# Performance work log

Hardware: AMD Instinct MI355X
Metric: run time of the kernel (lower is better)

The kernel has to match this reference:

```python
import jax, jax.numpy as jnp
import numpy as np
from jax import lax


def setup_inputs() -> dict:
    key = jax.random.key(0)
    k1, k2 = jax.random.split(key)
    B, C, H, W = 4, 32, 512, 512
    x = jax.random.normal(k1, (B, C, H, W), dtype=jnp.float32)
    # offset conv params: out_ch = 2*k*k = 18 (init: small weights, zero bias)
    w_off = jax.random.normal(k2, (18, C, 3, 3), dtype=jnp.float32) * 0.05
    b_off = jnp.zeros((18,), dtype=jnp.float32)
    return {"x": x, "w_off": w_off, "b_off": b_off}


def _grid_sample_bilinear_zeros(x, grid):
    # x: (B,C,H,W); grid: (B,H,W,2) in [-1,1], align_corners=True, zeros padding
    B, C, H, W = x.shape
    ix = (grid[..., 0] + 1.0) * 0.5 * (W - 1)  # (B,H,W)
    iy = (grid[..., 1] + 1.0) * 0.5 * (H - 1)
    x0 = jnp.floor(ix); y0 = jnp.floor(iy)
    x1 = x0 + 1.0;      y1 = y0 + 1.0
    wx1 = ix - x0; wx0 = 1.0 - wx1
    wy1 = iy - y0; wy0 = 1.0 - wy1
    bi = jnp.arange(B)[:, None, None]

    def corner(yc, xc, w):
        valid = (xc >= 0) & (xc <= W - 1) & (yc >= 0) & (yc <= H - 1)
        xi = jnp.clip(xc, 0, W - 1).astype(jnp.int32)
        yi = jnp.clip(yc, 0, H - 1).astype(jnp.int32)
        v = x[bi, :, yi, xi]  # (B,H,W,C)
        return v * (w * valid.astype(x.dtype))[..., None]

    out = (corner(y0, x0, wy0 * wx0) + corner(y0, x1, wy0 * wx1)
           + corner(y1, x0, wy1 * wx0) + corner(y1, x1, wy1 * wx1))
    return out.transpose(0, 3, 1, 2)  # (B,C,H,W)


def reference(x, w_off, b_off):
    B, C, H, W = x.shape
    # offset conv: 3x3, stride 1, padding 1 (shape-preserving)
    off = lax.conv_general_dilated(
        x, w_off, window_strides=(1, 1), padding=((1, 1), (1, 1)),
        dimension_numbers=("NCHW", "OIHW", "NCHW"))
    off = off + b_off[None, :, None, None]               # (B,18,H,W)
    off = off.transpose(0, 2, 3, 1).reshape(B, H, W, 9, 2)
    # base integer grid: (x, y) per pixel
    gy, gx = jnp.meshgrid(jnp.arange(H, dtype=x.dtype),
                          jnp.arange(W, dtype=x.dtype), indexing="ij")
    base = jnp.stack([gx, gy], axis=-1)                  # (H,W,2)
    g = base[None, :, :, None, :] + off                  # (B,H,W,9,2)
    g = g / jnp.array([W - 1, H - 1], dtype=x.dtype) * 2.0 - 1.0
    g = g[:, :, :, 0, :]                                 # only first kernel offset used
    return _grid_sample_bilinear_zeros(x, g)
```

## Files before the change

kernel.cpp:

```cpp
#include <hip/hip_runtime.h>

#define BB 4
#define CC 32
#define HH 512
#define WW 512
#define PLANE ((size_t)HH * WW)

typedef float fx4 __attribute__((ext_vector_type(4)));

__global__ __launch_bounds__(256) void deform_fused_kernel(
    const float* __restrict__ x, const float* __restrict__ w_off,
    const float* __restrict__ b_off, float* __restrict__ out) {
  const int nb = gridDim.x;
  const int i  = blockIdx.x;
  const int j  = (i & 7) * (nb >> 3) + (i >> 3);
  const int b    = j >> 8;
  const int row0 = (j & 255) << 1;

  const int t    = threadIdx.x;
  const int w4   = (t & 127) << 2;
  const int h    = row0 + (t >> 7);
  const int lane = t & 63;

  float4 a0v, a1v;
  a0v.x = a0v.y = a0v.z = a0v.w = b_off[0];
  a1v.x = a1v.y = a1v.z = a1v.w = b_off[1];

  const float* xb = x + (size_t)b * CC * PLANE + (size_t)h * WW + w4;

  float4 mA[3], mB[3];
  float  eA[3], eB[3];

  auto load_ch = [&](int ci, float4* m, float* e) {
#pragma unroll
    for (int r = 0; r < 3; ++r) {
      const int hy = h - 1 + r;
      const float* q = xb + (size_t)ci * PLANE + (ptrdiff_t)(r - 1) * WW;
      if (hy >= 0 && hy < HH) {
        m[r] = *(const float4*)q;
        const float* ea = (lane == 0) ? q - 1 : q + 4;
        const bool eok = (lane == 0) ? (w4 > 0)
                                     : (lane == 63 && w4 < WW - 4);
        e[r] = eok ? *ea : 0.f;
      } else {
        m[r].x = m[r].y = m[r].z = m[r].w = 0.f;
        e[r] = 0.f;
      }
    }
  };

  auto compute_ch = [&](int ci, const float4* m, const float* e) {
    const float* wp0 = w_off + ci * 9;
    const float* wp1 = w_off + 288 + ci * 9;
#pragma unroll
    for (int kh = 0; kh < 3; ++kh) {
      float vl = __shfl_up(m[kh].w, 1);
      if (lane == 0) vl = e[kh];
      float vr = __shfl_down(m[kh].x, 1);
      if (lane == 63) vr = e[kh];
      const float a0 = wp0[kh * 3 + 0], a1 = wp0[kh * 3 + 1], a2 = wp0[kh * 3 + 2];
      const float c0 = wp1[kh * 3 + 0], c1 = wp1[kh * 3 + 1], c2 = wp1[kh * 3 + 2];
      a0v.x += vl * a0 + m[kh].x * a1 + m[kh].y * a2;
      a0v.y += m[kh].x * a0 + m[kh].y * a1 + m[kh].z * a2;
      a0v.z += m[kh].y * a0 + m[kh].z * a1 + m[kh].w * a2;
      a0v.w += m[kh].z * a0 + m[kh].w * a1 + vr * a2;
      a1v.x += vl * c0 + m[kh].x * c1 + m[kh].y * c2;
      a1v.y += m[kh].x * c0 + m[kh].y * c1 + m[kh].z * c2;
      a1v.z += m[kh].y * c0 + m[kh].z * c1 + m[kh].w * c2;
      a1v.w += m[kh].z * c0 + m[kh].w * c1 + vr * c2;
    }
  };

  load_ch(0, mA, eA);
  for (int ci = 0; ci < CC - 2; ci += 2) {
    load_ch(ci + 1, mB, eB);
    compute_ch(ci, mA, eA);
    load_ch(ci + 2, mA, eA);
    compute_ch(ci + 1, mB, eB);
  }
  load_ch(CC - 1, mB, eB);
  compute_ch(CC - 2, mA, eA);
  compute_ch(CC - 1, mB, eB);

  float A0[4], A1[4], B0[4], B1[4];
  int   r0[4], r1[4];
  const float offx[4] = {a0v.x, a0v.y, a0v.z, a0v.w};
  const float offy[4] = {a1v.x, a1v.y, a1v.z, a1v.w};
#pragma unroll
  for (int p = 0; p < 4; ++p) {
    const float ix = (float)(w4 + p) + offx[p];
    const float iy = (float)h + offy[p];
    const float x0f = floorf(ix);
    const float y0f = floorf(iy);
    const float wx1 = ix - x0f, wx0 = 1.f - wx1;
    const float wy1 = iy - y0f, wy0 = 1.f - wy1;
    const bool vx0 = (x0f >= 0.f) && (x0f <= (float)(WW - 1));
    const bool vx1 = (x0f + 1.f >= 0.f) && (x0f + 1.f <= (float)(WW - 1));
    const bool vy0 = (y0f >= 0.f) && (y0f <= (float)(HH - 1));
    const bool vy1 = (y0f + 1.f >= 0.f) && (y0f + 1.f <= (float)(HH - 1));
    const int xi0 = (int)fminf(fmaxf(x0f, 0.f), (float)(WW - 1));
    const int xi1 = (int)fminf(fmaxf(x0f + 1.f, 0.f), (float)(WW - 1));
    const int yi0 = (int)fminf(fmaxf(y0f, 0.f), (float)(HH - 1));
    const int yi1 = (int)fminf(fmaxf(y0f + 1.f, 0.f), (float)(HH - 1));
    const float w00 = wy0 * wx0 * ((vy0 && vx0) ? 1.f : 0.f);
    const float w01 = wy0 * wx1 * ((vy0 && vx1) ? 1.f : 0.f);
    const float w10 = wy1 * wx0 * ((vy1 && vx0) ? 1.f : 0.f);
    const float w11 = wy1 * wx1 * ((vy1 && vx1) ? 1.f : 0.f);
    const int xL = (int)fminf(fmaxf(x0f, 0.f), (float)(WW - 2));
    const int s0 = (xi0 > xL) ? 1 : 0;
    const int s1 = (xi1 > xL) ? 1 : 0;
    A0[p] = (s0 ? 0.f : w00) + (s1 ? 0.f : w01);
    A1[p] = (s0 ? w00 : 0.f) + (s1 ? w01 : 0.f);
    B0[p] = (s0 ? 0.f : w10) + (s1 ? 0.f : w11);
    B1[p] = (s0 ? w10 : 0.f) + (s1 ? w11 : 0.f);
    r0[p] = yi0 * WW + xL;
    r1[p] = yi1 * WW + xL;
  }

  const float* xp = x + (size_t)b * CC * PLANE;
  float* ob = out + (size_t)b * CC * PLANE + (size_t)h * WW + w4;

#pragma unroll 1
  for (int cg = 0; cg < 8; ++cg) {
    float2 t0[4][4], t1[4][4];
    const float* pc = xp;
#pragma unroll
    for (int c = 0; c < 4; ++c) {
#pragma unroll
      for (int p = 0; p < 4; ++p) {
        __builtin_memcpy(&t0[c][p], pc + r0[p], 8);
        __builtin_memcpy(&t1[c][p], pc + r1[p], 8);
      }
      pc += PLANE;
    }
    float* o = ob;
#pragma unroll
    for (int c = 0; c < 4; ++c) {
      fx4 v;
      v.x = t0[c][0].x * A0[0] + t0[c][0].y * A1[0] + t1[c][0].x * B0[0] + t1[c][0].y * B1[0];
      v.y = t0[c][1].x * A0[1] + t0[c][1].y * A1[1] + t1[c][1].x * B0[1] + t1[c][1].y * B1[1];
      v.z = t0[c][2].x * A0[2] + t0[c][2].y * A1[2] + t1[c][2].x * B0[2] + t1[c][2].y * B1[2];
      v.w = t0[c][3].x * A0[3] + t0[c][3].y * A1[3] + t1[c][3].x * B0[3] + t1[c][3].y * B1[3];
      __builtin_nontemporal_store(v, (fx4*)o);
      o += PLANE;
    }
    xp += (size_t)4 * PLANE;
    ob += (size_t)4 * PLANE;
  }
}

extern "C" void kernel_launch(void* const* d_in, const int* in_sizes, int n_in,
                              void* d_out, int out_size, void* d_ws, size_t ws_size,
                              hipStream_t stream) {
  const float* x     = (const float*)d_in[0];
  const float* w_off = (const float*)d_in[1];
  const float* b_off = (const float*)d_in[2];
  float* out = (float*)d_out;

  deform_fused_kernel<<<1024, 256, 0, stream>>>(x, w_off, b_off, out);
}
```

Before: 298.4 us.

## Halve per-thread pixel work to two pixels and double block count

Each thread now handles 2 adjacent pixels instead of 4, and each 256-thread block covers one full row instead of two half-rows, with the grid doubled to 2048 blocks. A launch-bounds occupancy hint of 6 is added. The aim is lower register use and more waves in flight to hide gather latency. The cost is narrower float2 loads and stores, more wavefront-edge shuffles per pixel, and recomputed weight loads per block.

```diff
diff --git a/kernel.cpp b/kernel.cpp
--- a/kernel.cpp
+++ b/kernel.cpp
@@ -6,68 +6,63 @@
 #define WW 512
 #define PLANE ((size_t)HH * WW)
 
-typedef float fx4 __attribute__((ext_vector_type(4)));
+typedef float fx2 __attribute__((ext_vector_type(2)));
 
-__global__ __launch_bounds__(256) void deform_fused_kernel(
+__global__ __launch_bounds__(256, 6) void deform_fused_kernel(
     const float* __restrict__ x, const float* __restrict__ w_off,
     const float* __restrict__ b_off, float* __restrict__ out) {
   const int nb = gridDim.x;
   const int i  = blockIdx.x;
   const int j  = (i & 7) * (nb >> 3) + (i >> 3);
-  const int b    = j >> 8;
-  const int row0 = (j & 255) << 1;
+  const int b  = j >> 9;
+  const int h  = j & 511;
 
   const int t    = threadIdx.x;
-  const int w4   = (t & 127) << 2;
-  const int h    = row0 + (t >> 7);
+  const int w2   = t << 1;
   const int lane = t & 63;
 
-  float4 a0v, a1v;
-  a0v.x = a0v.y = a0v.z = a0v.w = b_off[0];
-  a1v.x = a1v.y = a1v.z = a1v.w = b_off[1];
+  float2 a0v, a1v;
+  a0v.x = a0v.y = b_off[0];
+  a1v.x = a1v.y = b_off[1];
 
-  const float* xb = x + (size_t)b * CC * PLANE + (size_t)h * WW + w4;
+  const float* xb = x + (size_t)b * CC * PLANE + (size_t)h * WW + w2;
 
-  float4 mA[3], mB[3];
+  float2 mA[3], mB[3];
   float  eA[3], eB[3];
 
-  auto load_ch = [&](int ci, float4* m, float* e) {
+  auto load_ch = [&](int ci, float2* m, float* e) {
 #pragma unroll
     for (int r = 0; r < 3; ++r) {
       const int hy = h - 1 + r;
       const float* q = xb + (size_t)ci * PLANE + (ptrdiff_t)(r - 1) * WW;
       if (hy >= 0 && hy < HH) {
-        m[r] = *(const float4*)q;
-        const float* ea = (lane == 0) ? q - 1 : q + 4;
-        const bool eok = (lane == 0) ? (w4 > 0)
-                                     : (lane == 63 && w4 < WW - 4);
+        m[r] = *(const float2*)q;
+        const float* ea = (lane == 0) ? q - 1 : q + 2;
+        const bool eok = (lane == 0) ? (w2 > 0)
+                                     : (lane == 63 && w2 < WW - 2);
         e[r] = eok ? *ea : 0.f;
       } else {
-        m[r].x = m[r].y = m[r].z = m[r].w = 0.f;
+        m[r].x = m[r].y = 0.f;
         e[r] = 0.f;
       }
     }
   };
 
-  auto compute_ch = [&](int ci, const float4* m, const float* e) {
+  auto compute_ch = [&](int ci, const float2* m, const float* e) {
     const float* wp0 = w_off + ci * 9;
     const float* wp1 = w_off + 288 + ci * 9;
 #pragma unroll
     for (int kh = 0; kh < 3; ++kh) {
-      float vl = __shfl_up(m[kh].w, 1);
+      float vl = __shfl_up(m[kh].y, 1);
       if (lane == 0) vl = e[kh];
       float vr = __shfl_down(m[kh].x, 1);
       if (lane == 63) vr = e[kh];
       const float a0 = wp0[kh * 3 + 0], a1 = wp0[kh * 3 + 1], a2 = wp0[kh * 3 + 2];
       const float c0 = wp1[kh * 3 + 0], c1 = wp1[kh * 3 + 1], c2 = wp1[kh * 3 + 2];
       a0v.x += vl * a0 + m[kh].x * a1 + m[kh].y * a2;
-      a0v.y += m[kh].x * a0 + m[kh].y * a1 + m[kh].z * a2;
-      a0v.z += m[kh].y * a0 + m[kh].z * a1 + m[kh].w * a2;
-      a0v.w += m[kh].z * a0 + m[kh].w * a1 + vr * a2;
+      a0v.y += m[kh].x * a0 + m[kh].y * a1 + vr * a2;
       a1v.x += vl * c0 + m[kh].x * c1 + m[kh].y * c2;
-      a1v.y += m[kh].x * c0 + m[kh].y * c1 + m[kh].z * c2;
-      a1v.z += m[kh].y * c0 + m[kh].z * c1 + m[kh].w * c2;
-      a1v.w += m[kh].z * c0 + m[kh].w * c1 + vr * c2;
+      a1v.y += m[kh].x * c0 + m[kh].y * c1 + vr * c2;
     }
   };
 
@@ -82,13 +77,13 @@
   compute_ch(CC - 2, mA, eA);
   compute_ch(CC - 1, mB, eB);
 
-  float A0[4], A1[4], B0[4], B1[4];
-  int   r0[4], r1[4];
-  const float offx[4] = {a0v.x, a0v.y, a0v.z, a0v.w};
-  const float offy[4] = {a1v.x, a1v.y, a1v.z, a1v.w};
+  float A0[2], A1[2], B0[2], B1[2];
+  int   r0[2], r1[2];
+  const float offx[2] = {a0v.x, a0v.y};
+  const float offy[2] = {a1v.x, a1v.y};
 #pragma unroll
-  for (int p = 0; p < 4; ++p) {
-    const float ix = (float)(w4 + p) + offx[p];
+  for (int p = 0; p < 2; ++p) {
+    const float ix = (float)(w2 + p) + offx[p];
     const float iy = (float)h + offy[p];
     const float x0f = floorf(ix);
     const float y0f = floorf(iy);
@@ -118,16 +113,16 @@
   }
 
   const float* xp = x + (size_t)b * CC * PLANE;
-  float* ob = out + (size_t)b * CC * PLANE + (size_t)h * WW + w4;
+  float* ob = out + (size_t)b * CC * PLANE + (size_t)h * WW + w2;
 
 #pragma unroll 1
   for (int cg = 0; cg < 8; ++cg) {
-    float2 t0[4][4], t1[4][4];
+    float2 t0[4][2], t1[4][2];
     const float* pc = xp;
 #pragma unroll
     for (int c = 0; c < 4; ++c) {
 #pragma unroll
-      for (int p = 0; p < 4; ++p) {
+      for (int p = 0; p < 2; ++p) {
         __builtin_memcpy(&t0[c][p], pc + r0[p], 8);
         __builtin_memcpy(&t1[c][p], pc + r1[p], 8);
       }
@@ -136,12 +131,10 @@
     float* o = ob;
 #pragma unroll
     for (int c = 0; c < 4; ++c) {
-      fx4 v;
+      fx2 v;
       v.x = t0[c][0].x * A0[0] + t0[c][0].y * A1[0] + t1[c][0].x * B0[0] + t1[c][0].y * B1[0];
       v.y = t0[c][1].x * A0[1] + t0[c][1].y * A1[1] + t1[c][1].x * B0[1] + t1[c][1].y * B1[1];
-      v.z = t0[c][2].x * A0[2] + t0[c][2].y * A1[2] + t1[c][2].x * B0[2] + t1[c][2].y * B1[2];
-      v.w = t0[c][3].x * A0[3] + t0[c][3].y * A1[3] + t1[c][3].x * B0[3] + t1[c][3].y * B1[3];
-      __builtin_nontemporal_store(v, (fx4*)o);
+      __builtin_nontemporal_store(v, (fx2*)o);
       o += PLANE;
     }
     xp += (size_t)4 * PLANE;
@@ -157,5 +150,5 @@
   const float* b_off = (const float*)d_in[2];
   float* out = (float*)d_out;
 
-  deform_fused_kernel<<<1024, 256, 0, stream>>>(x, w_off, b_off, out);
+  deform_fused_kernel<<<2048, 256, 0, stream>>>(x, w_off, b_off, out);
 }
```

After: 286.2 us. 1.04x faster.
